# Performance work log

Measured on AMD Instinct MI355X. Metric: run time of the kernel, lower is better.

The kernel has to match this reference:

```python
import jax, jax.numpy as jnp
import numpy as np

E, K = 8, 2            # num_experts, top_k
D, H = 1024, 4096      # d_model, expert_hidden_dim
B, S = 4, 2048         # batch, seq
AUX_W = 0.01


def setup_inputs() -> dict:
    key = jax.random.key(0)
    k0, k1, k2, k3 = jax.random.split(key, 4)
    return {
        "x": jax.random.normal(k0, (B, S, D), jnp.float32),
        "router_w": jax.random.normal(k1, (D, E), jnp.float32) * 0.02,  # normal(0.02) init per MoERouter
        "router_b": jnp.zeros((E,), jnp.float32),
        "w_up": jax.random.normal(k2, (E, D, H), jnp.float32) * (1.0 / np.sqrt(D)),
        "b_up": jnp.zeros((E, H), jnp.float32),
        "w_down": jax.random.normal(k3, (E, H, D), jnp.float32) * (1.0 / np.sqrt(H)),
        "b_down": jnp.zeros((E, D), jnp.float32),
    }


def reference(x, router_w, router_b, w_up, b_up, w_down, b_down):
    # Router
    logits = x @ router_w + router_b                       # (B,S,E)
    router_probs = jax.nn.softmax(logits, axis=-1)         # (B,S,E)
    topk_logits, topk_idx = jax.lax.top_k(logits, K)       # (B,S,K)
    topk_p = jax.nn.softmax(topk_logits, axis=-1)          # (B,S,K)

    # Dense all-expert MLP (matches original: every expert computed on every token)
    h = jax.nn.gelu(jnp.einsum('bsd,edh->bseh', x, w_up) + b_up)   # (B,S,E,H)
    all_out = jnp.einsum('bseh,ehd->bsed', h, w_down) + b_down     # (B,S,E,D)

    # Top-k gather + weighted combine
    sel = jnp.take_along_axis(all_out, topk_idx[..., None], axis=2)  # (B,S,K,D)
    output = jnp.sum(topk_p[..., None] * sel, axis=2)                # (B,S,D)

    # Load-balancing aux loss (Switch/Mixtral formulation)
    counts = jnp.zeros((E,), jnp.float32).at[topk_idx.reshape(-1)].add(1.0)
    fraction = counts / (B * S * K)
    prob_mean = router_probs.mean(axis=(0, 1))
    aux_loss = E * jnp.sum(fraction * prob_mean) * AUX_W
    return output, aux_loss, router_probs
```

## Files before the change

kernel.cpp:

```cpp
#include <hip/hip_runtime.h>
#include <hip/hip_bf16.h>
#include <stdint.h>

constexpr int NT = 8192;
constexpr int NE = 8;
constexpr int ND = 1024;
constexpr int NH = 4096;

typedef __attribute__((ext_vector_type(8))) short short8;
typedef __attribute__((ext_vector_type(4))) float f32x4;

constexpr size_t O_XBF  = 0;
constexpr size_t O_WUPT = O_XBF  + (size_t)NT * ND * 2;
constexpr size_t O_WDNT = O_WUPT + (size_t)NE * NH * ND * 2;
constexpr size_t O_HBUF = O_WDNT + (size_t)NE * ND * NH * 2;
constexpr size_t O_STOK = O_HBUF + (size_t)NT * 2 * NH * 2;
constexpr size_t O_SP   = O_STOK + (size_t)NT * 2 * 4;
constexpr size_t O_TKE  = O_SP   + (size_t)NT * 2 * 4;
constexpr size_t O_TKP  = O_TKE  + (size_t)NT * 2 * 4;
constexpr size_t O_CTRL = O_TKP  + (size_t)NT * 2 * 4;

__device__ __forceinline__ void gl_lds16(const void* g, void* l) {
  using GP = char __attribute__((address_space(1))) *;
  using LP = char __attribute__((address_space(3))) *;
  __builtin_amdgcn_global_load_lds((GP)(uintptr_t)g, (LP)(uint32_t)(uintptr_t)l, 16, 0, 0);
}

__device__ __forceinline__ float fast_gelu(float x) {
  float u  = 0.7978845608028654f * (x + 0.044715f * x * x * x);
  float ex = __expf(2.0f * u);
  float th = 1.0f - 2.0f / (ex + 1.0f);
  return 0.5f * x * (1.0f + th);
}

__global__ __launch_bounds__(256) void moe_router(
    const float* __restrict__ x, const float* __restrict__ rw, const float* __restrict__ rb,
    __hip_bfloat16* __restrict__ xbf,
    float* __restrict__ probs_out, int* __restrict__ topk_e, float* __restrict__ topk_p,
    int* __restrict__ cnt_ek, float* __restrict__ probsum)
{
  __shared__ float ps[NE];
  __shared__ int cs[16];
  const int tid = threadIdx.x;
  if (tid < NE) ps[tid] = 0.f;
  if (tid < 16) cs[tid] = 0;
  __syncthreads();
  const int lane = tid & 63, wv = tid >> 6;
  for (int it = 0; it < 8; ++it) {
    const int t = blockIdx.x * 4 + wv + it * 1024;
    const float* xr = x + (size_t)t * ND;
    float acc[NE] = {};
#pragma unroll 4
    for (int j = 0; j < 16; ++j) {
      const int d = j * 64 + lane;
      const float xv = xr[d];
      xbf[(size_t)t * ND + d] = __float2bfloat16(xv);
      const float* w = rw + (size_t)d * NE;
#pragma unroll
      for (int ee = 0; ee < NE; ++ee) acc[ee] += xv * w[ee];
    }
#pragma unroll
    for (int ee = 0; ee < NE; ++ee)
#pragma unroll
      for (int off = 32; off >= 1; off >>= 1)
        acc[ee] += __shfl_down(acc[ee], off, 64);
    if (lane == 0) {
      float lg[NE];
#pragma unroll
      for (int ee = 0; ee < NE; ++ee) lg[ee] = acc[ee] + rb[ee];
      float mx = lg[0];
#pragma unroll
      for (int ee = 1; ee < NE; ++ee) mx = fmaxf(mx, lg[ee]);
      float s = 0.f, pe[NE];
#pragma unroll
      for (int ee = 0; ee < NE; ++ee) { pe[ee] = __expf(lg[ee] - mx); s += pe[ee]; }
      const float inv = 1.f / s;
#pragma unroll
      for (int ee = 0; ee < NE; ++ee) {
        const float pr = pe[ee] * inv;
        probs_out[(size_t)t * NE + ee] = pr;
        atomicAdd(&ps[ee], pr);
      }
      int i1 = 0; float l1 = lg[0];
#pragma unroll
      for (int ee = 1; ee < NE; ++ee) if (lg[ee] > l1) { l1 = lg[ee]; i1 = ee; }
      int i2 = 0; float l2 = -3.0e38f;
#pragma unroll
      for (int ee = 0; ee < NE; ++ee) if (ee != i1 && lg[ee] > l2) { l2 = lg[ee]; i2 = ee; }
      const float e2 = __expf(l2 - l1);
      const float dn = 1.f + e2;
      topk_e[t * 2]     = i1;  topk_e[t * 2 + 1] = i2;
      topk_p[t * 2]     = 1.f / dn;
      topk_p[t * 2 + 1] = e2 / dn;
      atomicAdd(&cs[i1 * 2], 1);
      atomicAdd(&cs[i2 * 2 + 1], 1);
    }
  }
  __syncthreads();
  if (tid < NE) atomicAdd(&probsum[tid], ps[tid]);
  if (tid < 16) atomicAdd(&cnt_ek[tid], cs[tid]);
}

__global__ void moe_finalize(const int* __restrict__ cnt_ek, int* __restrict__ off_ek,
                             const float* __restrict__ probsum, float* __restrict__ aux_out)
{
  if (threadIdx.x == 0 && blockIdx.x == 0) {
    int run = 0;
    for (int i = 0; i < 16; ++i) { off_ek[i] = run; run += cnt_ek[i]; }
    float aux = 0.f;
    for (int ee = 0; ee < NE; ++ee) {
      float frac = (float)(cnt_ek[2 * ee] + cnt_ek[2 * ee + 1]) / (float)(NT * 2);
      aux += frac * (probsum[ee] / (float)NT);
    }
    aux_out[0] = (float)NE * aux * 0.01f;
  }
}

__global__ __launch_bounds__(256) void moe_scatter(
    const int* __restrict__ topk_e, const float* __restrict__ topk_p,
    const int* __restrict__ off_ek, int* __restrict__ fill_ek,
    int* __restrict__ slot_token, float* __restrict__ slot_p)
{
  const int t = blockIdx.x * 256 + threadIdx.x;
  if (t >= NT) return;
#pragma unroll
  for (int k = 0; k < 2; ++k) {
    const int ee = topk_e[t * 2 + k];
    const int id = ee * 2 + k;
    const int r = atomicAdd(&fill_ek[id], 1);
    const int slot = off_ek[id] + r;
    slot_token[slot] = t;
    slot_p[slot] = topk_p[t * 2 + k];
  }
}

__global__ __launch_bounds__(256) void moe_transpose_cast(
    const float* __restrict__ in, __hip_bfloat16* __restrict__ outp, int Adim, int Bdim)
{
  __shared__ float tile[64][65];
  const int e = blockIdx.z;
  const int b0 = blockIdx.x * 64, a0 = blockIdx.y * 64;
  const float* ip = in + (size_t)e * Adim * Bdim + (size_t)a0 * Bdim + b0;
  const int c = threadIdx.x & 63, r4 = threadIdx.x >> 6;
#pragma unroll
  for (int i = 0; i < 16; ++i) {
    const int r = r4 * 16 + i;
    tile[r][c] = ip[(size_t)r * Bdim + c];
  }
  __syncthreads();
  __hip_bfloat16* op = outp + (size_t)e * Bdim * Adim + (size_t)b0 * Adim + a0;
  const int rr = threadIdx.x & 63, c4 = threadIdx.x >> 6;
#pragma unroll
  for (int i = 0; i < 16; ++i) {
    const int cc = c4 * 16 + i;
    op[(size_t)cc * Adim + rr] = __float2bfloat16(tile[rr][cc]);
  }
}

__global__ __launch_bounds__(256, 2) void moe_gemm_up(
    const __hip_bfloat16* __restrict__ xbf,
    const __hip_bfloat16* __restrict__ wupT,
    const float* __restrict__ b_up,
    const int* __restrict__ slot_token,
    const int* __restrict__ cnt_ek, const int* __restrict__ off_ek,
    __hip_bfloat16* __restrict__ hbuf)
{
  const int e = blockIdx.z;
  const int cnt = cnt_ek[2 * e] + cnt_ek[2 * e + 1];
  const int m0 = blockIdx.y * 128;
  if (m0 >= cnt) return;
  const int base = off_ek[2 * e];
  const int n0 = blockIdx.x * 128;
  const int valid = (cnt - m0 < 128) ? (cnt - m0) : 128;

  __shared__ __align__(16) __hip_bfloat16 As[128 * 32];
  __shared__ __align__(16) __hip_bfloat16 Bs[128 * 32];

  const int tid = threadIdx.x;
  const int lane = tid & 63, wv = tid >> 6;

  const int c0 = tid, c1 = 256 + tid;
  const int ra0 = c0 >> 2, ra1 = c1 >> 2;
  const int kc0 = (((c0 & 3) ^ ((ra0 >> 1) & 3))) * 8;
  const int kc1 = (((c1 & 3) ^ ((ra1 >> 1) & 3))) * 8;
  const int sa0 = base + ((m0 + ra0 < cnt) ? (m0 + ra0) : (cnt - 1));
  const int sa1 = base + ((m0 + ra1 < cnt) ? (m0 + ra1) : (cnt - 1));
  const __hip_bfloat16* ga0 = xbf + (size_t)slot_token[sa0] * ND + kc0;
  const __hip_bfloat16* ga1 = xbf + (size_t)slot_token[sa1] * ND + kc1;
  const __hip_bfloat16* gb0 = wupT + ((size_t)e * NH + n0 + ra0) * ND + kc0;
  const __hip_bfloat16* gb1 = wupT + ((size_t)e * NH + n0 + ra1) * ND + kc1;
  char* lA0 = (char*)As + c0 * 16;  char* lA1 = (char*)As + c1 * 16;
  char* lB0 = (char*)Bs + c0 * 16;  char* lB1 = (char*)Bs + c1 * 16;

  const int wm = (wv >> 1) * 64, wn = (wv & 1) * 64;
  const int l15 = lane & 15, q = lane >> 4;
  const int ssw = (q ^ ((l15 >> 1) & 3)) * 16;
  const char* rA = (const char*)As + (wm + l15) * 64 + ssw;
  const char* rB = (const char*)Bs + (wn + l15) * 64 + ssw;

  f32x4 acc[4][4] = {};

  for (int kk = 0; kk < ND; kk += 32) {
    __syncthreads();
    gl_lds16(ga0 + kk, lA0);
    gl_lds16(ga1 + kk, lA1);
    gl_lds16(gb0 + kk, lB0);
    gl_lds16(gb1 + kk, lB1);
    __syncthreads();
    short8 af[4], bfr[4];
#pragma unroll
    for (int i = 0; i < 4; ++i) af[i]  = *(const short8*)(rA + i * 1024);
#pragma unroll
    for (int i = 0; i < 4; ++i) bfr[i] = *(const short8*)(rB + i * 1024);
#pragma unroll
    for (int mt = 0; mt < 4; ++mt)
#pragma unroll
      for (int nt = 0; nt < 4; ++nt)
        acc[mt][nt] = __builtin_amdgcn_mfma_f32_16x16x32_bf16(af[mt], bfr[nt], acc[mt][nt], 0, 0, 0);
  }

#pragma unroll
  for (int mt = 0; mt < 4; ++mt) {
#pragma unroll
    for (int rr = 0; rr < 4; ++rr) {
      const int row = wm + mt * 16 + q * 4 + rr;
      if (row < valid) {
        const size_t rbase = (size_t)(base + m0 + row) * NH;
#pragma unroll
        for (int nt = 0; nt < 4; ++nt) {
          const int col = n0 + wn + nt * 16 + l15;
          const float v = acc[mt][nt][rr] + b_up[e * NH + col];
          hbuf[rbase + col] = __float2bfloat16(fast_gelu(v));
        }
      }
    }
  }
}

__global__ __launch_bounds__(256, 2) void moe_gemm_down(
    const __hip_bfloat16* __restrict__ hbuf,
    const __hip_bfloat16* __restrict__ wdnT,
    const float* __restrict__ b_down,
    const int* __restrict__ slot_token, const float* __restrict__ slot_p,
    const int* __restrict__ cnt_ek, const int* __restrict__ off_ek,
    float* __restrict__ out, int kpos)
{
  const int e = blockIdx.z;
  const int id = 2 * e + kpos;
  const int cnt = cnt_ek[id];
  const int m0 = blockIdx.y * 128;
  if (m0 >= cnt) return;
  const int base = off_ek[id];
  const int n0 = blockIdx.x * 128;
  const int valid = (cnt - m0 < 128) ? (cnt - m0) : 128;

  __shared__ __align__(16) __hip_bfloat16 As[128 * 32];
  __shared__ __align__(16) __hip_bfloat16 Bs[128 * 32];

  const int tid = threadIdx.x;
  const int lane = tid & 63, wv = tid >> 6;

  const int c0 = tid, c1 = 256 + tid;
  const int ra0 = c0 >> 2, ra1 = c1 >> 2;
  const int kc0 = (((c0 & 3) ^ ((ra0 >> 1) & 3))) * 8;
  const int kc1 = (((c1 & 3) ^ ((ra1 >> 1) & 3))) * 8;
  const int sa0 = base + ((m0 + ra0 < cnt) ? (m0 + ra0) : (cnt - 1));
  const int sa1 = base + ((m0 + ra1 < cnt) ? (m0 + ra1) : (cnt - 1));
  const __hip_bfloat16* ga0 = hbuf + (size_t)sa0 * NH + kc0;
  const __hip_bfloat16* ga1 = hbuf + (size_t)sa1 * NH + kc1;
  const __hip_bfloat16* gb0 = wdnT + ((size_t)e * ND + n0 + ra0) * NH + kc0;
  const __hip_bfloat16* gb1 = wdnT + ((size_t)e * ND + n0 + ra1) * NH + kc1;
  char* lA0 = (char*)As + c0 * 16;  char* lA1 = (char*)As + c1 * 16;
  char* lB0 = (char*)Bs + c0 * 16;  char* lB1 = (char*)Bs + c1 * 16;

  const int wm = (wv >> 1) * 64, wn = (wv & 1) * 64;
  const int l15 = lane & 15, q = lane >> 4;
  const int ssw = (q ^ ((l15 >> 1) & 3)) * 16;
  const char* rA = (const char*)As + (wm + l15) * 64 + ssw;
  const char* rB = (const char*)Bs + (wn + l15) * 64 + ssw;

  f32x4 acc[4][4] = {};

  for (int kk = 0; kk < NH; kk += 32) {
    __syncthreads();
    gl_lds16(ga0 + kk, lA0);
    gl_lds16(ga1 + kk, lA1);
    gl_lds16(gb0 + kk, lB0);
    gl_lds16(gb1 + kk, lB1);
    __syncthreads();
    short8 af[4], bfr[4];
#pragma unroll
    for (int i = 0; i < 4; ++i) af[i]  = *(const short8*)(rA + i * 1024);
#pragma unroll
    for (int i = 0; i < 4; ++i) bfr[i] = *(const short8*)(rB + i * 1024);
#pragma unroll
    for (int mt = 0; mt < 4; ++mt)
#pragma unroll
      for (int nt = 0; nt < 4; ++nt)
        acc[mt][nt] = __builtin_amdgcn_mfma_f32_16x16x32_bf16(af[mt], bfr[nt], acc[mt][nt], 0, 0, 0);
  }

#pragma unroll
  for (int mt = 0; mt < 4; ++mt) {
#pragma unroll
    for (int rr = 0; rr < 4; ++rr) {
      const int row = wm + mt * 16 + q * 4 + rr;
      if (row < valid) {
        const int slot = base + m0 + row;
        const int tok = slot_token[slot];
        const float p = slot_p[slot];
        const size_t obase = (size_t)tok * ND;
#pragma unroll
        for (int nt = 0; nt < 4; ++nt) {
          const int col = n0 + wn + nt * 16 + l15;
          const float v = (acc[mt][nt][rr] + b_down[e * ND + col]) * p;
          if (kpos == 0) out[obase + col] = v;
          else           out[obase + col] += v;
        }
      }
    }
  }
}

extern "C" void kernel_launch(void* const* d_in, const int* in_sizes, int n_in,
                              void* d_out, int out_size, void* d_ws, size_t ws_size,
                              hipStream_t stream) {
  (void)in_sizes; (void)n_in; (void)out_size; (void)ws_size;
  const float* x   = (const float*)d_in[0];
  const float* rw  = (const float*)d_in[1];
  const float* rb  = (const float*)d_in[2];
  const float* wup = (const float*)d_in[3];
  const float* bup = (const float*)d_in[4];
  const float* wdn = (const float*)d_in[5];
  const float* bdn = (const float*)d_in[6];
  float* out = (float*)d_out;

  char* ws = (char*)d_ws;
  __hip_bfloat16* xbf  = (__hip_bfloat16*)(ws + O_XBF);
  __hip_bfloat16* wupT = (__hip_bfloat16*)(ws + O_WUPT);
  __hip_bfloat16* wdnT = (__hip_bfloat16*)(ws + O_WDNT);
  __hip_bfloat16* hbuf = (__hip_bfloat16*)(ws + O_HBUF);
  int*   slot_token = (int*)(ws + O_STOK);
  float* slot_p     = (float*)(ws + O_SP);
  int*   topk_e     = (int*)(ws + O_TKE);
  float* topk_p     = (float*)(ws + O_TKP);
  int*   cnt_ek  = (int*)(ws + O_CTRL);
  int*   fill_ek = (int*)(ws + O_CTRL + 64);
  float* probsum = (float*)(ws + O_CTRL + 128);
  int*   off_ek  = (int*)(ws + O_CTRL + 192);

  hipMemsetAsync(ws + O_CTRL, 0, 256, stream);

  moe_transpose_cast<<<dim3(NH / 64, ND / 64, NE), 256, 0, stream>>>(wup, wupT, ND, NH);
  moe_transpose_cast<<<dim3(ND / 64, NH / 64, NE), 256, 0, stream>>>(wdn, wdnT, NH, ND);

  moe_router<<<256, 256, 0, stream>>>(x, rw, rb, xbf, out + (size_t)NT * ND + 1,
                                      topk_e, topk_p, cnt_ek, probsum);
  moe_finalize<<<1, 64, 0, stream>>>(cnt_ek, off_ek, probsum, out + (size_t)NT * ND);
  moe_scatter<<<NT / 256, 256, 0, stream>>>(topk_e, topk_p, off_ek, fill_ek, slot_token, slot_p);

  moe_gemm_up<<<dim3(NH / 128, 64, NE), 256, 0, stream>>>(xbf, wupT, bup, slot_token,
                                                          cnt_ek, off_ek, hbuf);
  moe_gemm_down<<<dim3(ND / 128, 64, NE), 256, 0, stream>>>(hbuf, wdnT, bdn, slot_token, slot_p,
                                                            cnt_ek, off_ek, out, 0);
  moe_gemm_down<<<dim3(ND / 128, 64, NE), 256, 0, stream>>>(hbuf, wdnT, bdn, slot_token, slot_p,
                                                            cnt_ek, off_ek, out, 1);
}
```

Before: 1.022 ms.

## Compact expert tile lists, use 512-thread GEMM blocks, vectorize weight transpose-cast

```diff
diff --git a/kernel.cpp b/kernel.cpp
--- a/kernel.cpp
+++ b/kernel.cpp
@@ -19,6 +19,8 @@
 constexpr size_t O_TKE  = O_SP   + (size_t)NT * 2 * 4;
 constexpr size_t O_TKP  = O_TKE  + (size_t)NT * 2 * 4;
 constexpr size_t O_CTRL = O_TKP  + (size_t)NT * 2 * 4;
+constexpr size_t O_TLUP = O_CTRL + 272;
+constexpr size_t O_TLDN = O_TLUP + 144 * 4;
 
 __device__ __forceinline__ void gl_lds16(const void* g, void* l) {
   using GP = char __attribute__((address_space(1))) *;
@@ -102,7 +104,9 @@
 }
 
 __global__ void moe_finalize(const int* __restrict__ cnt_ek, int* __restrict__ off_ek,
-                             const float* __restrict__ probsum, float* __restrict__ aux_out)
+                             const float* __restrict__ probsum, float* __restrict__ aux_out,
+                             int* __restrict__ ntiles, int* __restrict__ tl_up,
+                             int* __restrict__ tl_dn)
 {
   if (threadIdx.x == 0 && blockIdx.x == 0) {
     int run = 0;
@@ -113,6 +117,20 @@
       aux += frac * (probsum[ee] / (float)NT);
     }
     aux_out[0] = (float)NE * aux * 0.01f;
+    int ntu = 0;
+    for (int e = 0; e < NE; ++e) {
+      const int c = cnt_ek[2 * e] + cnt_ek[2 * e + 1];
+      for (int mb = 0; mb < (c + 127) / 128; ++mb) tl_up[ntu++] = (e << 16) | mb;
+    }
+    ntiles[0] = ntu;
+    for (int kp = 0; kp < 2; ++kp) {
+      int nt = 0;
+      for (int e = 0; e < NE; ++e) {
+        const int c = cnt_ek[2 * e + kp];
+        for (int mb = 0; mb < (c + 127) / 128; ++mb) tl_dn[kp * 80 + nt++] = (e << 16) | mb;
+      }
+      ntiles[1 + kp] = nt;
+    }
   }
 }
 
@@ -137,39 +155,49 @@
 __global__ __launch_bounds__(256) void moe_transpose_cast(
     const float* __restrict__ in, __hip_bfloat16* __restrict__ outp, int Adim, int Bdim)
 {
-  __shared__ float tile[64][65];
+  __shared__ unsigned short tile[64 * 66];
   const int e = blockIdx.z;
   const int b0 = blockIdx.x * 64, a0 = blockIdx.y * 64;
   const float* ip = in + (size_t)e * Adim * Bdim + (size_t)a0 * Bdim + b0;
-  const int c = threadIdx.x & 63, r4 = threadIdx.x >> 6;
-#pragma unroll
-  for (int i = 0; i < 16; ++i) {
-    const int r = r4 * 16 + i;
-    tile[r][c] = ip[(size_t)r * Bdim + c];
+  const int c4 = (threadIdx.x & 15) * 4;
+  const int r0 = threadIdx.x >> 4;
+#pragma unroll
+  for (int i = 0; i < 4; ++i) {
+    const int r = r0 + i * 16;
+    const float4 v = *(const float4*)(ip + (size_t)r * Bdim + c4);
+    ushort4 u;
+    u.x = __hip_bfloat16_raw(__float2bfloat16(v.x)).x;
+    u.y = __hip_bfloat16_raw(__float2bfloat16(v.y)).x;
+    u.z = __hip_bfloat16_raw(__float2bfloat16(v.z)).x;
+    u.w = __hip_bfloat16_raw(__float2bfloat16(v.w)).x;
+    *(ushort4*)&tile[r * 66 + c4] = u;
   }
   __syncthreads();
-  __hip_bfloat16* op = outp + (size_t)e * Bdim * Adim + (size_t)b0 * Adim + a0;
-  const int rr = threadIdx.x & 63, c4 = threadIdx.x >> 6;
-#pragma unroll
-  for (int i = 0; i < 16; ++i) {
-    const int cc = c4 * 16 + i;
-    op[(size_t)cc * Adim + rr] = __float2bfloat16(tile[rr][cc]);
-  }
-}
-
-__global__ __launch_bounds__(256, 2) void moe_gemm_up(
+  unsigned short* op = (unsigned short*)outp + (size_t)e * Bdim * Adim + (size_t)b0 * Adim + a0;
+  const int cc  = threadIdx.x >> 2;
+  const int rr0 = (threadIdx.x & 3) * 16;
+  unsigned short u[16];
+#pragma unroll
+  for (int i = 0; i < 16; ++i) u[i] = tile[(rr0 + i) * 66 + cc];
+  *(short8*)(op + (size_t)cc * Adim + rr0)     = *(short8*)&u[0];
+  *(short8*)(op + (size_t)cc * Adim + rr0 + 8) = *(short8*)&u[8];
+}
+
+__global__ __launch_bounds__(512, 5) void moe_gemm_up(
     const __hip_bfloat16* __restrict__ xbf,
     const __hip_bfloat16* __restrict__ wupT,
     const float* __restrict__ b_up,
     const int* __restrict__ slot_token,
     const int* __restrict__ cnt_ek, const int* __restrict__ off_ek,
+    const int* __restrict__ ntiles, const int* __restrict__ tl_up,
     __hip_bfloat16* __restrict__ hbuf)
 {
-  const int e = blockIdx.z;
+  if ((int)blockIdx.y >= ntiles[0]) return;
+  const int tl = tl_up[blockIdx.y];
+  const int e = tl >> 16, mb = tl & 0xffff;
   const int cnt = cnt_ek[2 * e] + cnt_ek[2 * e + 1];
-  const int m0 = blockIdx.y * 128;
-  if (m0 >= cnt) return;
   const int base = off_ek[2 * e];
+  const int m0 = mb * 128;
   const int n0 = blockIdx.x * 128;
   const int valid = (cnt - m0 < 128) ? (cnt - m0) : 128;
 
@@ -179,43 +207,36 @@
   const int tid = threadIdx.x;
   const int lane = tid & 63, wv = tid >> 6;
 
-  const int c0 = tid, c1 = 256 + tid;
-  const int ra0 = c0 >> 2, ra1 = c1 >> 2;
-  const int kc0 = (((c0 & 3) ^ ((ra0 >> 1) & 3))) * 8;
-  const int kc1 = (((c1 & 3) ^ ((ra1 >> 1) & 3))) * 8;
-  const int sa0 = base + ((m0 + ra0 < cnt) ? (m0 + ra0) : (cnt - 1));
-  const int sa1 = base + ((m0 + ra1 < cnt) ? (m0 + ra1) : (cnt - 1));
-  const __hip_bfloat16* ga0 = xbf + (size_t)slot_token[sa0] * ND + kc0;
-  const __hip_bfloat16* ga1 = xbf + (size_t)slot_token[sa1] * ND + kc1;
-  const __hip_bfloat16* gb0 = wupT + ((size_t)e * NH + n0 + ra0) * ND + kc0;
-  const __hip_bfloat16* gb1 = wupT + ((size_t)e * NH + n0 + ra1) * ND + kc1;
-  char* lA0 = (char*)As + c0 * 16;  char* lA1 = (char*)As + c1 * 16;
-  char* lB0 = (char*)Bs + c0 * 16;  char* lB1 = (char*)Bs + c1 * 16;
-
-  const int wm = (wv >> 1) * 64, wn = (wv & 1) * 64;
+  const int ra = tid >> 2;
+  const int kc = ((tid & 3) ^ ((ra >> 1) & 3)) * 8;
+  const int sa = base + ((m0 + ra < cnt) ? (m0 + ra) : (cnt - 1));
+  const __hip_bfloat16* ga = xbf + (size_t)slot_token[sa] * ND + kc;
+  const __hip_bfloat16* gb = wupT + ((size_t)e * NH + n0 + ra) * ND + kc;
+  char* lA = (char*)As + tid * 16;
+  char* lB = (char*)Bs + tid * 16;
+
+  const int wm = (wv >> 2) * 64, wn = (wv & 3) * 32;
   const int l15 = lane & 15, q = lane >> 4;
   const int ssw = (q ^ ((l15 >> 1) & 3)) * 16;
   const char* rA = (const char*)As + (wm + l15) * 64 + ssw;
   const char* rB = (const char*)Bs + (wn + l15) * 64 + ssw;
 
-  f32x4 acc[4][4] = {};
+  f32x4 acc[4][2] = {};
 
   for (int kk = 0; kk < ND; kk += 32) {
     __syncthreads();
-    gl_lds16(ga0 + kk, lA0);
-    gl_lds16(ga1 + kk, lA1);
-    gl_lds16(gb0 + kk, lB0);
-    gl_lds16(gb1 + kk, lB1);
+    gl_lds16(ga + kk, lA);
+    gl_lds16(gb + kk, lB);
     __syncthreads();
-    short8 af[4], bfr[4];
+    short8 af[4], bfr[2];
 #pragma unroll
     for (int i = 0; i < 4; ++i) af[i]  = *(const short8*)(rA + i * 1024);
 #pragma unroll
-    for (int i = 0; i < 4; ++i) bfr[i] = *(const short8*)(rB + i * 1024);
+    for (int i = 0; i < 2; ++i) bfr[i] = *(const short8*)(rB + i * 1024);
 #pragma unroll
     for (int mt = 0; mt < 4; ++mt)
 #pragma unroll
-      for (int nt = 0; nt < 4; ++nt)
+      for (int nt = 0; nt < 2; ++nt)
         acc[mt][nt] = __builtin_amdgcn_mfma_f32_16x16x32_bf16(af[mt], bfr[nt], acc[mt][nt], 0, 0, 0);
   }
 
@@ -227,7 +248,7 @@
       if (row < valid) {
         const size_t rbase = (size_t)(base + m0 + row) * NH;
 #pragma unroll
-        for (int nt = 0; nt < 4; ++nt) {
+        for (int nt = 0; nt < 2; ++nt) {
           const int col = n0 + wn + nt * 16 + l15;
           const float v = acc[mt][nt][rr] + b_up[e * NH + col];
           hbuf[rbase + col] = __float2bfloat16(fast_gelu(v));
@@ -237,20 +258,22 @@
   }
 }
 
-__global__ __launch_bounds__(256, 2) void moe_gemm_down(
+__global__ __launch_bounds__(512, 5) void moe_gemm_down(
     const __hip_bfloat16* __restrict__ hbuf,
     const __hip_bfloat16* __restrict__ wdnT,
     const float* __restrict__ b_down,
     const int* __restrict__ slot_token, const float* __restrict__ slot_p,
     const int* __restrict__ cnt_ek, const int* __restrict__ off_ek,
+    const int* __restrict__ ntiles, const int* __restrict__ tl_dn,
     float* __restrict__ out, int kpos)
 {
-  const int e = blockIdx.z;
+  if ((int)blockIdx.y >= ntiles[1 + kpos]) return;
+  const int tl = tl_dn[kpos * 80 + blockIdx.y];
+  const int e = tl >> 16, mb = tl & 0xffff;
   const int id = 2 * e + kpos;
   const int cnt = cnt_ek[id];
-  const int m0 = blockIdx.y * 128;
-  if (m0 >= cnt) return;
   const int base = off_ek[id];
+  const int m0 = mb * 128;
   const int n0 = blockIdx.x * 128;
   const int valid = (cnt - m0 < 128) ? (cnt - m0) : 128;
 
@@ -260,43 +283,36 @@
   const int tid = threadIdx.x;
   const int lane = tid & 63, wv = tid >> 6;
 
-  const int c0 = tid, c1 = 256 + tid;
-  const int ra0 = c0 >> 2, ra1 = c1 >> 2;
-  const int kc0 = (((c0 & 3) ^ ((ra0 >> 1) & 3))) * 8;
-  const int kc1 = (((c1 & 3) ^ ((ra1 >> 1) & 3))) * 8;
-  const int sa0 = base + ((m0 + ra0 < cnt) ? (m0 + ra0) : (cnt - 1));
-  const int sa1 = base + ((m0 + ra1 < cnt) ? (m0 + ra1) : (cnt - 1));
-  const __hip_bfloat16* ga0 = hbuf + (size_t)sa0 * NH + kc0;
-  const __hip_bfloat16* ga1 = hbuf + (size_t)sa1 * NH + kc1;
-  const __hip_bfloat16* gb0 = wdnT + ((size_t)e * ND + n0 + ra0) * NH + kc0;
-  const __hip_bfloat16* gb1 = wdnT + ((size_t)e * ND + n0 + ra1) * NH + kc1;
-  char* lA0 = (char*)As + c0 * 16;  char* lA1 = (char*)As + c1 * 16;
-  char* lB0 = (char*)Bs + c0 * 16;  char* lB1 = (char*)Bs + c1 * 16;
-
-  const int wm = (wv >> 1) * 64, wn = (wv & 1) * 64;
+  const int ra = tid >> 2;
+  const int kc = ((tid & 3) ^ ((ra >> 1) & 3)) * 8;
+  const int sa = base + ((m0 + ra < cnt) ? (m0 + ra) : (cnt - 1));
+  const __hip_bfloat16* ga = hbuf + (size_t)sa * NH + kc;
+  const __hip_bfloat16* gb = wdnT + ((size_t)e * ND + n0 + ra) * NH + kc;
+  char* lA = (char*)As + tid * 16;
+  char* lB = (char*)Bs + tid * 16;
+
+  const int wm = (wv >> 2) * 64, wn = (wv & 3) * 32;
   const int l15 = lane & 15, q = lane >> 4;
   const int ssw = (q ^ ((l15 >> 1) & 3)) * 16;
   const char* rA = (const char*)As + (wm + l15) * 64 + ssw;
   const char* rB = (const char*)Bs + (wn + l15) * 64 + ssw;
 
-  f32x4 acc[4][4] = {};
+  f32x4 acc[4][2] = {};
 
   for (int kk = 0; kk < NH; kk += 32) {
     __syncthreads();
-    gl_lds16(ga0 + kk, lA0);
-    gl_lds16(ga1 + kk, lA1);
-    gl_lds16(gb0 + kk, lB0);
-    gl_lds16(gb1 + kk, lB1);
+    gl_lds16(ga + kk, lA);
+    gl_lds16(gb + kk, lB);
     __syncthreads();
-    short8 af[4], bfr[4];
+    short8 af[4], bfr[2];
 #pragma unroll
     for (int i = 0; i < 4; ++i) af[i]  = *(const short8*)(rA + i * 1024);
 #pragma unroll
-    for (int i = 0; i < 4; ++i) bfr[i] = *(const short8*)(rB + i * 1024);
+    for (int i = 0; i < 2; ++i) bfr[i] = *(const short8*)(rB + i * 1024);
 #pragma unroll
     for (int mt = 0; mt < 4; ++mt)
 #pragma unroll
-      for (int nt = 0; nt < 4; ++nt)
+      for (int nt = 0; nt < 2; ++nt)
         acc[mt][nt] = __builtin_amdgcn_mfma_f32_16x16x32_bf16(af[mt], bfr[nt], acc[mt][nt], 0, 0, 0);
   }
 
@@ -311,7 +327,7 @@
         const float p = slot_p[slot];
         const size_t obase = (size_t)tok * ND;
 #pragma unroll
-        for (int nt = 0; nt < 4; ++nt) {
+        for (int nt = 0; nt < 2; ++nt) {
           const int col = n0 + wn + nt * 16 + l15;
           const float v = (acc[mt][nt][rr] + b_down[e * ND + col]) * p;
           if (kpos == 0) out[obase + col] = v;
@@ -348,21 +364,25 @@
   int*   fill_ek = (int*)(ws + O_CTRL + 64);
   float* probsum = (float*)(ws + O_CTRL + 128);
   int*   off_ek  = (int*)(ws + O_CTRL + 192);
-
-  hipMemsetAsync(ws + O_CTRL, 0, 256, stream);
+  int*   ntiles  = (int*)(ws + O_CTRL + 256);
+  int*   tl_up   = (int*)(ws + O_TLUP);
+  int*   tl_dn   = (int*)(ws + O_TLDN);
+
+  hipMemsetAsync(ws + O_CTRL, 0, 272, stream);
 
   moe_transpose_cast<<<dim3(NH / 64, ND / 64, NE), 256, 0, stream>>>(wup, wupT, ND, NH);
   moe_transpose_cast<<<dim3(ND / 64, NH / 64, NE), 256, 0, stream>>>(wdn, wdnT, NH, ND);
 
   moe_router<<<256, 256, 0, stream>>>(x, rw, rb, xbf, out + (size_t)NT * ND + 1,
                                       topk_e, topk_p, cnt_ek, probsum);
-  moe_finalize<<<1, 64, 0, stream>>>(cnt_ek, off_ek, probsum, out + (size_t)NT * ND);
+  moe_finalize<<<1, 64, 0, stream>>>(cnt_ek, off_ek, probsum, out + (size_t)NT * ND,
+                                     ntiles, tl_up, tl_dn);
   moe_scatter<<<NT / 256, 256, 0, stream>>>(topk_e, topk_p, off_ek, fill_ek, slot_token, slot_p);
 
-  moe_gemm_up<<<dim3(NH / 128, 64, NE), 256, 0, stream>>>(xbf, wupT, bup, slot_token,
-                                                          cnt_ek, off_ek, hbuf);
-  moe_gemm_down<<<dim3(ND / 128, 64, NE), 256, 0, stream>>>(hbuf, wdnT, bdn, slot_token, slot_p,
-                                                            cnt_ek, off_ek, out, 0);
-  moe_gemm_down<<<dim3(ND / 128, 64, NE), 256, 0, stream>>>(hbuf, wdnT, bdn, slot_token, slot_p,
-                                                            cnt_ek, off_ek, out, 1);
-}
+  moe_gemm_up<<<dim3(NH / 128, 144, 1), 512, 0, stream>>>(xbf, wupT, bup, slot_token,
+                                                          cnt_ek, off_ek, ntiles, tl_up, hbuf);
+  moe_gemm_down<<<dim3(ND / 128, 80, 1), 512, 0, stream>>>(hbuf, wdnT, bdn, slot_token, slot_p,
+                                                           cnt_ek, off_ek, ntiles, tl_dn, out, 0);
+  moe_gemm_down<<<dim3(ND / 128, 80, 1), 512, 0, stream>>>(hbuf, wdnT, bdn, slot_token, slot_p,
+                                                           cnt_ek, off_ek, ntiles, tl_dn, out, 1);
+}
```

Result: faster. 933.2 us (-8.7%).
